# Performance work log

Hardware: AMD Instinct MI355X
Metric: run time of the kernel (lower is better)

Reference implementation:

```python
import jax, jax.numpy as jnp
import numpy as np
import math

D_MODEL = 1024
HEAD_DIM = 256
GAMMA = 0.9


def setup_inputs() -> dict:
    key = jax.random.key(0)
    k1, k2, k3, k4 = jax.random.split(key, 4)
    B, L = 4, 4096
    x = jax.random.normal(k1, (B, L, D_MODEL), dtype=jnp.float32)
    s = 1.0 / math.sqrt(D_MODEL)
    W_Q = jax.random.normal(k2, (HEAD_DIM, D_MODEL), dtype=jnp.float32) * s
    W_K = jax.random.normal(k3, (HEAD_DIM, D_MODEL), dtype=jnp.float32) * s
    W_V = jax.random.normal(k4, (HEAD_DIM, D_MODEL), dtype=jnp.float32) * s
    return {"x": x, "W_Q": W_Q, "W_K": W_K, "W_V": W_V}


def _decay_mask(L: int, gamma: float) -> jnp.ndarray:
    # D[i,j] = gamma^(i-j) if i >= j else 0
    idx = jnp.arange(L)
    diff = idx[:, None] - idx[None, :]
    return jnp.where(diff >= 0, jnp.power(jnp.float32(gamma), diff.astype(jnp.float32)), 0.0)


def reference(x, W_Q, W_K, W_V):
    B, L, _ = x.shape
    Q = jnp.einsum('bld,hd->blh', x, W_Q)  # (B,L,H)
    K = jnp.einsum('bld,hd->blh', x, W_K)
    V = jnp.einsum('bld,hd->blh', x, W_V)
    D = _decay_mask(L, GAMMA)  # (L,L)
    scores = jnp.einsum('bih,bjh->bij', Q, K) * D[None, :, :]
    scores = scores / jnp.sqrt(jnp.float32(HEAD_DIM))
    return jnp.einsum('bij,bjh->bih', scores, V)  # (B,L,H)
```

## Files before the change

### kernel.cpp

```cpp
#include <hip/hip_runtime.h>

typedef unsigned short u16;
typedef unsigned int u32;
typedef __attribute__((ext_vector_type(8))) short bf16x8;
typedef __attribute__((ext_vector_type(4))) float f32x4;
typedef __attribute__((ext_vector_type(4))) unsigned short u16x4;

#define DEVI __device__ __forceinline__

constexpr float L2GAMMA = -0.15200309344504997f;
constexpr float INV_SQRT_H = 0.0625f;

DEVI u16 f2bf(float x) {
  union { float f; unsigned u; } v; v.f = x;
  unsigned r = v.u + 0x7FFFu + ((v.u >> 16) & 1u);
  return (u16)(r >> 16);
}

DEVI u32 pack2bf(float f0, float f1) {
  u32 u0 = __float_as_uint(f0) + 0x8000u;
  u32 u1 = __float_as_uint(f1) + 0x8000u;
  return __builtin_amdgcn_perm(u1, u0, 0x07060302u);
}

__global__ void cvt_w_kernel(const float4* __restrict__ wq, const float4* __restrict__ wk,
                             const float4* __restrict__ wv, u16x4* __restrict__ dst) {
  int i = blockIdx.x * blockDim.x + threadIdx.x;
  int w = i >> 16, off = i & 65535;
  const float4* s = (w == 0) ? wq : ((w == 1) ? wk : wv);
  float4 v = s[off];
  u16x4 o; o.x = f2bf(v.x); o.y = f2bf(v.y); o.z = f2bf(v.z); o.w = f2bf(v.w);
  dst[(w << 16) + off] = o;
}

__global__ __launch_bounds__(512, 2) void qkv_gemm_kernel(const float* __restrict__ Xf, const u16* __restrict__ Wb,
                                                          u16* __restrict__ Qb, u16* __restrict__ Kb,
                                                          u16* __restrict__ Vt) {
  __shared__ u16 Alds[2][256 * 32];
  __shared__ u16 Blds[2][192 * 32];
  const int bid = blockIdx.x;
  const int xcd = bid & 7, seq = bid >> 3;
  const int m0 = (xcd * 8 + (seq >> 2)) * 256;
  const int n0 = (seq & 3) * 192;
  const int tid = threadIdx.x;
  const int wid = tid >> 6, lane = tid & 63;
  const int wm = wid >> 1, wn = wid & 1;
  const int lrow = lane & 15, lkg = lane >> 4;
  const int kidx = (lrow & 3) ^ ((lrow >> 2) & 3);
  const int kw = ((tid >> 2) & 3) ^ ((tid >> 4) & 3);
  const int kb = ((lane >> 2) & 3) ^ ((lane >> 4) & 3);

  const float* agbase = Xf + (size_t)(m0 + (tid >> 2)) * 1024 + (tid & 3) * 8;
  const int awr0 = (tid >> 2) * 32 + (((tid & 3) ^ kw) << 3);
  const int awr1 = awr0 + 128 * 32;
  float4 ar[4];

  const u16* bgbase = Wb + (size_t)(n0 + wid * 16 + (lane >> 2)) * 1024 + (((lane & 3) ^ kb) << 3);

#define LOADA(KT) do { const float* g_ = agbase + (KT) * 32; \
  ar[0] = *(const float4*)(g_); \
  ar[1] = *(const float4*)(g_ + 4); \
  ar[2] = *(const float4*)(g_ + (size_t)128 * 1024); \
  ar[3] = *(const float4*)(g_ + (size_t)128 * 1024 + 4); } while (0)

#define STAGEB(KT, BUF) do { const u16* gB_ = bgbase + (KT) * 32; \
  __builtin_amdgcn_global_load_lds((const __attribute__((address_space(1))) void*)gB_, \
      (__attribute__((address_space(3))) void*)&Blds[BUF][wid * 512], 16, 0, 0); \
  if (wid < 4) { \
    __builtin_amdgcn_global_load_lds((const __attribute__((address_space(1))) void*)(gB_ + (size_t)128 * 1024), \
        (__attribute__((address_space(3))) void*)&Blds[BUF][(8 + wid) * 512], 16, 0, 0); } } while (0)

#define CVTWRITE(BUF) do { \
  uint4 p0_, p1_; \
  p0_.x = pack2bf(ar[0].x, ar[0].y); p0_.y = pack2bf(ar[0].z, ar[0].w); \
  p0_.z = pack2bf(ar[1].x, ar[1].y); p0_.w = pack2bf(ar[1].z, ar[1].w); \
  p1_.x = pack2bf(ar[2].x, ar[2].y); p1_.y = pack2bf(ar[2].z, ar[2].w); \
  p1_.z = pack2bf(ar[3].x, ar[3].y); p1_.w = pack2bf(ar[3].z, ar[3].w); \
  *(uint4*)&Alds[BUF][awr0] = p0_; \
  *(uint4*)&Alds[BUF][awr1] = p1_; } while (0)

  f32x4 acc[4][6] = {};

  LOADA(0);
  STAGEB(0, 0);
  CVTWRITE(0);
  __syncthreads();

  for (int kt = 0; kt < 32; ++kt) {
    const int p = kt & 1;
    if (kt < 31) { LOADA(kt + 1); STAGEB(kt + 1, p ^ 1); }
    const u16* Ab = Alds[p];
    const u16* Bb = Blds[p];
    bf16x8 af[4], bfr[6];
    const int sw = (lkg ^ kidx) << 3;
#pragma unroll
    for (int mf = 0; mf < 4; ++mf) af[mf] = *(const bf16x8*)&Ab[(wm * 64 + mf * 16 + lrow) * 32 + sw];
#pragma unroll
    for (int nf = 0; nf < 6; ++nf) bfr[nf] = *(const bf16x8*)&Bb[(wn * 96 + nf * 16 + lrow) * 32 + sw];
    __builtin_amdgcn_s_setprio(1);
#pragma unroll
    for (int mf = 0; mf < 4; ++mf)
#pragma unroll
      for (int nf = 0; nf < 6; ++nf)
        acc[mf][nf] = __builtin_amdgcn_mfma_f32_16x16x32_bf16(af[mf], bfr[nf], acc[mf][nf], 0, 0, 0);
    __builtin_amdgcn_s_setprio(0);
    if (kt < 31) CVTWRITE(p ^ 1);
    __syncthreads();
  }

#pragma unroll
  for (int mf = 0; mf < 4; ++mf)
#pragma unroll
    for (int nf = 0; nf < 6; ++nf) {
      const int gm = m0 + wm * 64 + mf * 16 + lkg * 4;
      const int c = n0 + wn * 96 + nf * 16 + lrow;
      if (c < 512) {
        u16* Dst = (c < 256) ? Qb : Kb;
        const int cc = c & 255;
#pragma unroll
        for (int r = 0; r < 4; ++r) Dst[(size_t)(gm + r) * 256 + cc] = f2bf(acc[mf][nf][r]);
      } else {
        const int h = c - 512;
        const int bb = gm >> 12, l = gm & 4095;
        u16x4 pk;
        pk.x = f2bf(acc[mf][nf][0]); pk.y = f2bf(acc[mf][nf][1]);
        pk.z = f2bf(acc[mf][nf][2]); pk.w = f2bf(acc[mf][nf][3]);
        *(u16x4*)&Vt[((size_t)bb * 256 + h) * 4096 + l] = pk;
      }
    }
}

__global__ __launch_bounds__(256) void attn_kernel(const u16* __restrict__ Qb, const u16* __restrict__ Kb,
                                                   const u16* __restrict__ Vt, float* __restrict__ out) {
  __shared__ u16 Plds[32 * 72];
  const int raw = blockIdx.x;
  const int aid = (raw & 7) * 64 + (raw >> 3);
  const int b = aid >> 7;
  const int qt = aid & 127;
  const int qb = qt * 32;
  const int tid = threadIdx.x;
  const int wid = tid >> 6, lane = tid & 63;
  const int lrow = lane & 15, lkg = lane >> 4, lk = lkg * 8;
  const size_t bQK = (size_t)b * 4096 * 256;

  bf16x8 qf[2][8];
#pragma unroll
  for (int mf = 0; mf < 2; ++mf) {
    const u16* Qrow = Qb + bQK + (size_t)(qb + mf * 16 + lrow) * 256;
#pragma unroll
    for (int kf = 0; kf < 8; ++kf) qf[mf][kf] = *(const bf16x8*)&Qrow[kf * 32 + lk];
  }

  int kstart = qb - 256; if (kstart < 0) kstart = 0; kstart &= ~63;
  const int njt = (qb + 32 - kstart + 63) >> 6;

  f32x4 oacc[2][4] = {};

  for (int jt = 0; jt < njt; ++jt) {
    const int kb = kstart + jt * 64;
    f32x4 s[2] = {};
    const u16* Krow = Kb + bQK + (size_t)(kb + wid * 16 + lrow) * 256;
#pragma unroll
    for (int kf = 0; kf < 8; ++kf) {
      const bf16x8 kfr = *(const bf16x8*)&Krow[kf * 32 + lk];
      s[0] = __builtin_amdgcn_mfma_f32_16x16x32_bf16(qf[0][kf], kfr, s[0], 0, 0, 0);
      s[1] = __builtin_amdgcn_mfma_f32_16x16x32_bf16(qf[1][kf], kfr, s[1], 0, 0, 0);
    }
    const int kg = kb + wid * 16 + lrow;
#pragma unroll
    for (int mf = 0; mf < 2; ++mf) {
      const int qg = qb + mf * 16 + lkg * 4;
#pragma unroll
      for (int r = 0; r < 4; ++r) {
        const int d = qg + r - kg;
        const float pv = (d >= 0) ? s[mf][r] * exp2f((float)d * L2GAMMA) * INV_SQRT_H : 0.0f;
        Plds[(mf * 16 + lkg * 4 + r) * 72 + wid * 16 + lrow] = f2bf(pv);
      }
    }
    __syncthreads();
#pragma unroll
    for (int ks = 0; ks < 2; ++ks) {
      bf16x8 pa[2];
      pa[0] = *(const bf16x8*)&Plds[(lrow) * 72 + ks * 32 + lk];
      pa[1] = *(const bf16x8*)&Plds[(16 + lrow) * 72 + ks * 32 + lk];
#pragma unroll
      for (int nf = 0; nf < 4; ++nf) {
        const bf16x8 vb = *(const bf16x8*)&Vt[((size_t)b * 256 + wid * 64 + nf * 16 + lrow) * 4096 + kb + ks * 32 + lk];
        oacc[0][nf] = __builtin_amdgcn_mfma_f32_16x16x32_bf16(pa[0], vb, oacc[0][nf], 0, 0, 0);
        oacc[1][nf] = __builtin_amdgcn_mfma_f32_16x16x32_bf16(pa[1], vb, oacc[1][nf], 0, 0, 0);
      }
    }
    __syncthreads();
  }

#pragma unroll
  for (int mf = 0; mf < 2; ++mf) {
    float* obase = out + ((size_t)b * 4096 + qb + mf * 16 + lkg * 4) * 256 + wid * 64 + lrow;
#pragma unroll
    for (int nf = 0; nf < 4; ++nf)
#pragma unroll
      for (int r = 0; r < 4; ++r)
        obase[(size_t)r * 256 + nf * 16] = oacc[mf][nf][r];
  }
}

extern "C" void kernel_launch(void* const* d_in, const int* in_sizes, int n_in,
                              void* d_out, int out_size, void* d_ws, size_t ws_size,
                              hipStream_t stream) {
  const float* x  = (const float*)d_in[0];
  const float* wq = (const float*)d_in[1];
  const float* wk = (const float*)d_in[2];
  const float* wv = (const float*)d_in[3];
  float* out = (float*)d_out;
  char* ws = (char*)d_ws;
  u16* Wb = (u16*)(ws);
  u16* Qb = (u16*)(ws + (size_t)1572864);
  u16* Kb = (u16*)(ws + (size_t)9961472);
  u16* Vt = (u16*)(ws + (size_t)18350080);

  hipLaunchKernelGGL(cvt_w_kernel, dim3(768), dim3(256), 0, stream,
                     (const float4*)wq, (const float4*)wk, (const float4*)wv, (u16x4*)Wb);
  hipLaunchKernelGGL(qkv_gemm_kernel, dim3(256), dim3(512), 0, stream, x, Wb, Qb, Kb, Vt);
  hipLaunchKernelGGL(attn_kernel, dim3(512), dim3(256), 0, stream, Qb, Kb, Vt, out);
}
```

Baseline: 84.58 us.

## Retile QKV GEMM to 256x256 tiles with 4-stage LDS ring pipeline

The QKV projection GEMM moves from 256x192 output tiles (256 blocks) to 256x256 tiles (192 blocks), so each block produces exactly one of Q, K or V. The LDS double buffer becomes a 4-deep ring with two register sets for the fp32 X loads, keeping loads two to four k-steps ahead, and uses explicit vmcnt/lgkmcnt waits plus raw s_barrier instead of __syncthreads. The intent is to hide global-load latency better and raise MFMA work per LDS read. In exchange it uses 128KB of LDS, which limits occupancy to one block per CU, and launches fewer blocks than there are CUs.

```diff
diff --git a/kernel.cpp b/kernel.cpp
--- a/kernel.cpp
+++ b/kernel.cpp
@@ -36,98 +36,113 @@
 __global__ __launch_bounds__(512, 2) void qkv_gemm_kernel(const float* __restrict__ Xf, const u16* __restrict__ Wb,
                                                           u16* __restrict__ Qb, u16* __restrict__ Kb,
                                                           u16* __restrict__ Vt) {
-  __shared__ u16 Alds[2][256 * 32];
-  __shared__ u16 Blds[2][192 * 32];
-  const int bid = blockIdx.x;
-  const int xcd = bid & 7, seq = bid >> 3;
-  const int m0 = (xcd * 8 + (seq >> 2)) * 256;
-  const int n0 = (seq & 3) * 192;
+  __shared__ u16 lds[4][16384];
+  const int raw = blockIdx.x;
+  const int xcd = raw & 7, idx = raw >> 3;
+  const int m0 = (xcd * 8 + idx / 3) * 256;
+  const int nt = idx % 3;
+  const int n0 = nt * 256;
   const int tid = threadIdx.x;
   const int wid = tid >> 6, lane = tid & 63;
-  const int wm = wid >> 1, wn = wid & 1;
+  const int wm = wid >> 2, wn = wid & 3;
   const int lrow = lane & 15, lkg = lane >> 4;
-  const int kidx = (lrow & 3) ^ ((lrow >> 2) & 3);
-  const int kw = ((tid >> 2) & 3) ^ ((tid >> 4) & 3);
-  const int kb = ((lane >> 2) & 3) ^ ((lane >> 4) & 3);
-
-  const float* agbase = Xf + (size_t)(m0 + (tid >> 2)) * 1024 + (tid & 3) * 8;
-  const int awr0 = (tid >> 2) * 32 + (((tid & 3) ^ kw) << 3);
-  const int awr1 = awr0 + 128 * 32;
-  float4 ar[4];
-
-  const u16* bgbase = Wb + (size_t)(n0 + wid * 16 + (lane >> 2)) * 1024 + (((lane & 3) ^ kb) << 3);
-
-#define LOADA(KT) do { const float* g_ = agbase + (KT) * 32; \
-  ar[0] = *(const float4*)(g_); \
-  ar[1] = *(const float4*)(g_ + 4); \
-  ar[2] = *(const float4*)(g_ + (size_t)128 * 1024); \
-  ar[3] = *(const float4*)(g_ + (size_t)128 * 1024 + 4); } while (0)
-
-#define STAGEB(KT, BUF) do { const u16* gB_ = bgbase + (KT) * 32; \
-  __builtin_amdgcn_global_load_lds((const __attribute__((address_space(1))) void*)gB_, \
-      (__attribute__((address_space(3))) void*)&Blds[BUF][wid * 512], 16, 0, 0); \
-  if (wid < 4) { \
-    __builtin_amdgcn_global_load_lds((const __attribute__((address_space(1))) void*)(gB_ + (size_t)128 * 1024), \
-        (__attribute__((address_space(3))) void*)&Blds[BUF][(8 + wid) * 512], 16, 0, 0); } } while (0)
-
-#define CVTWRITE(BUF) do { \
-  uint4 p0_, p1_; \
-  p0_.x = pack2bf(ar[0].x, ar[0].y); p0_.y = pack2bf(ar[0].z, ar[0].w); \
-  p0_.z = pack2bf(ar[1].x, ar[1].y); p0_.w = pack2bf(ar[1].z, ar[1].w); \
-  p1_.x = pack2bf(ar[2].x, ar[2].y); p1_.y = pack2bf(ar[2].z, ar[2].w); \
-  p1_.z = pack2bf(ar[3].x, ar[3].y); p1_.w = pack2bf(ar[3].z, ar[3].w); \
-  *(uint4*)&Alds[BUF][awr0] = p0_; \
-  *(uint4*)&Alds[BUF][awr1] = p1_; } while (0)
-
-  f32x4 acc[4][6] = {};
-
-  LOADA(0);
-  STAGEB(0, 0);
-  CVTWRITE(0);
-  __syncthreads();
-
-  for (int kt = 0; kt < 32; ++kt) {
-    const int p = kt & 1;
-    if (kt < 31) { LOADA(kt + 1); STAGEB(kt + 1, p ^ 1); }
-    const u16* Ab = Alds[p];
-    const u16* Bb = Blds[p];
-    bf16x8 af[4], bfr[6];
-    const int sw = (lkg ^ kidx) << 3;
-#pragma unroll
-    for (int mf = 0; mf < 4; ++mf) af[mf] = *(const bf16x8*)&Ab[(wm * 64 + mf * 16 + lrow) * 32 + sw];
-#pragma unroll
-    for (int nf = 0; nf < 6; ++nf) bfr[nf] = *(const bf16x8*)&Bb[(wn * 96 + nf * 16 + lrow) * 32 + sw];
-    __builtin_amdgcn_s_setprio(1);
-#pragma unroll
-    for (int mf = 0; mf < 4; ++mf)
-#pragma unroll
-      for (int nf = 0; nf < 6; ++nf)
-        acc[mf][nf] = __builtin_amdgcn_mfma_f32_16x16x32_bf16(af[mf], bfr[nf], acc[mf][nf], 0, 0, 0);
-    __builtin_amdgcn_s_setprio(0);
-    if (kt < 31) CVTWRITE(p ^ 1);
-    __syncthreads();
-  }
-
-#pragma unroll
-  for (int mf = 0; mf < 4; ++mf)
-#pragma unroll
-    for (int nf = 0; nf < 6; ++nf) {
-      const int gm = m0 + wm * 64 + mf * 16 + lkg * 4;
-      const int c = n0 + wn * 96 + nf * 16 + lrow;
-      if (c < 512) {
-        u16* Dst = (c < 256) ? Qb : Kb;
-        const int cc = c & 255;
-#pragma unroll
-        for (int r = 0; r < 4; ++r) Dst[(size_t)(gm + r) * 256 + cc] = f2bf(acc[mf][nf][r]);
-      } else {
-        const int h = c - 512;
+
+#define STAGEB(T, BUF) do { const int k0_ = (T) * 32; \
+  _Pragma("unroll") for (int i_ = 0; i_ < 2; ++i_) { \
+    const int p_ = tid + i_ * 512; \
+    const int row_ = p_ >> 2; \
+    const int sc_ = ((p_ & 3) ^ ((p_ >> 4) & 3)) << 3; \
+    const u16* g_ = Wb + (size_t)(n0 + row_) * 1024 + k0_ + sc_; \
+    __builtin_amdgcn_global_load_lds((const __attribute__((address_space(1))) void*)g_, \
+        (__attribute__((address_space(3))) void*)&lds[BUF][8192 + p_ * 8], 16, 0, 0); } } while (0)
+
+#define LOADA(T, R) do { const int k0_ = (T) * 32; \
+  _Pragma("unroll") for (int i_ = 0; i_ < 2; ++i_) { \
+    const int p_ = tid + i_ * 512; \
+    const int row_ = p_ >> 2; \
+    const int sc_ = ((p_ & 3) ^ ((p_ >> 4) & 3)) << 3; \
+    const float* g_ = Xf + (size_t)(m0 + row_) * 1024 + k0_ + sc_; \
+    R[2 * i_]     = *(const float4*)g_; \
+    R[2 * i_ + 1] = *(const float4*)(g_ + 4); } } while (0)
+
+#define CVTWRITE(R, BUF) do { \
+  _Pragma("unroll") for (int i_ = 0; i_ < 2; ++i_) { \
+    const int p_ = tid + i_ * 512; \
+    uint4 pk_; \
+    pk_.x = pack2bf(R[2 * i_].x, R[2 * i_].y); \
+    pk_.y = pack2bf(R[2 * i_].z, R[2 * i_].w); \
+    pk_.z = pack2bf(R[2 * i_ + 1].x, R[2 * i_ + 1].y); \
+    pk_.w = pack2bf(R[2 * i_ + 1].z, R[2 * i_ + 1].w); \
+    *(uint4*)&lds[BUF][p_ * 8] = pk_; } } while (0)
+
+  f32x4 acc[8][4] = {};
+  float4 arE[4], arO[4];
+
+  LOADA(0, arE); LOADA(1, arO);
+  STAGEB(0, 0);  STAGEB(1, 1);
+  CVTWRITE(arE, 0); LOADA(2, arE);
+  CVTWRITE(arO, 1); LOADA(3, arO);
+  asm volatile("s_waitcnt vmcnt(8)" ::: "memory");
+  asm volatile("s_waitcnt lgkmcnt(0)" ::: "memory");
+  __builtin_amdgcn_s_barrier();
+  __builtin_amdgcn_sched_barrier(0);
+
+#define BODY(T, AR) do { \
+  const int t_ = (T); \
+  const int rb_ = t_ & 3; \
+  if (t_ + 2 < 32) STAGEB(t_ + 2, (t_ + 2) & 3); \
+  bf16x8 af_[8], bf_[4]; \
+  { const u16* Ab_ = &lds[rb_][0]; const u16* Bb_ = &lds[rb_][8192]; \
+    const int sw_ = (lkg ^ ((lrow >> 2) & 3)) << 3; \
+    _Pragma("unroll") for (int mf = 0; mf < 8; ++mf) \
+      af_[mf] = *(const bf16x8*)&Ab_[(wm * 128 + mf * 16 + lrow) * 32 + sw_]; \
+    _Pragma("unroll") for (int nf = 0; nf < 4; ++nf) \
+      bf_[nf] = *(const bf16x8*)&Bb_[(wn * 64 + nf * 16 + lrow) * 32 + sw_]; } \
+  __builtin_amdgcn_s_setprio(1); \
+  _Pragma("unroll") for (int mf = 0; mf < 8; ++mf) \
+    _Pragma("unroll") for (int nf = 0; nf < 4; ++nf) \
+      acc[mf][nf] = __builtin_amdgcn_mfma_f32_16x16x32_bf16(af_[mf], bf_[nf], acc[mf][nf], 0, 0, 0); \
+  __builtin_amdgcn_s_setprio(0); \
+  if (t_ <= 28)      { asm volatile("s_waitcnt vmcnt(6)" ::: "memory"); } \
+  else if (t_ == 29) { asm volatile("s_waitcnt vmcnt(2)" ::: "memory"); } \
+  else               { asm volatile("s_waitcnt vmcnt(0)" ::: "memory"); } \
+  if (t_ + 2 < 32) { CVTWRITE(AR, (t_ + 2) & 3); } \
+  if (t_ + 4 < 32) { LOADA(t_ + 4, AR); } \
+  asm volatile("s_waitcnt lgkmcnt(0)" ::: "memory"); \
+  __builtin_amdgcn_s_barrier(); \
+  __builtin_amdgcn_sched_barrier(0); \
+} while (0)
+
+  for (int ti = 0; ti < 16; ++ti) {
+    BODY(2 * ti, arE);
+    BODY(2 * ti + 1, arO);
+  }
+
+  if (nt < 2) {
+    u16* Dst = (nt == 0) ? Qb : Kb;
+#pragma unroll
+    for (int mf = 0; mf < 8; ++mf)
+#pragma unroll
+      for (int nf = 0; nf < 4; ++nf) {
+        const int gm = m0 + wm * 128 + mf * 16 + lkg * 4;
+        const int c = wn * 64 + nf * 16 + lrow;
+#pragma unroll
+        for (int r = 0; r < 4; ++r) Dst[(size_t)(gm + r) * 256 + c] = f2bf(acc[mf][nf][r]);
+      }
+  } else {
+#pragma unroll
+    for (int mf = 0; mf < 8; ++mf)
+#pragma unroll
+      for (int nf = 0; nf < 4; ++nf) {
+        const int gm = m0 + wm * 128 + mf * 16 + lkg * 4;
+        const int h = wn * 64 + nf * 16 + lrow;
         const int bb = gm >> 12, l = gm & 4095;
         u16x4 pk;
         pk.x = f2bf(acc[mf][nf][0]); pk.y = f2bf(acc[mf][nf][1]);
         pk.z = f2bf(acc[mf][nf][2]); pk.w = f2bf(acc[mf][nf][3]);
         *(u16x4*)&Vt[((size_t)bb * 256 + h) * 4096 + l] = pk;
       }
-    }
+  }
 }
 
 __global__ __launch_bounds__(256) void attn_kernel(const u16* __restrict__ Qb, const u16* __restrict__ Kb,
@@ -220,6 +235,6 @@
 
   hipLaunchKernelGGL(cvt_w_kernel, dim3(768), dim3(256), 0, stream,
                      (const float4*)wq, (const float4*)wk, (const float4*)wv, (u16x4*)Wb);
-  hipLaunchKernelGGL(qkv_gemm_kernel, dim3(256), dim3(512), 0, stream, x, Wb, Qb, Kb, Vt);
+  hipLaunchKernelGGL(qkv_gemm_kernel, dim3(192), dim3(512), 0, stream, x, Wb, Qb, Kb, Vt);
   hipLaunchKernelGGL(attn_kernel, dim3(512), dim3(256), 0, stream, Qb, Kb, Vt, out);
 }
```

Result: slower. 87.95 us (+4.0%).

## Retile QKV GEMM to 64-row blocks covering all 768 columns with triple-buffered weights

Applied to the files above, without the earlier changes.

The QKV projection GEMM now gives each block 64 rows of X and all 768 output columns, so every X element is read and converted to bf16 once instead of four times. Weight tiles are staged through a three-deep LDS ring using global_load_lds, with explicit vmcnt/lgkmcnt waits and a single barrier per k-step instead of __syncthreads. The cost is that every block now streams the full 1.5MB bf16 weight matrix, which puts more load on L2. The larger LDS footprint may also lower occupancy.

```diff
diff --git a/kernel.cpp b/kernel.cpp
--- a/kernel.cpp
+++ b/kernel.cpp
@@ -36,84 +36,88 @@
 __global__ __launch_bounds__(512, 2) void qkv_gemm_kernel(const float* __restrict__ Xf, const u16* __restrict__ Wb,
                                                           u16* __restrict__ Qb, u16* __restrict__ Kb,
                                                           u16* __restrict__ Vt) {
-  __shared__ u16 Alds[2][256 * 32];
-  __shared__ u16 Blds[2][192 * 32];
+  __shared__ u16 Blds[3][24576];
+  __shared__ u16 Alds[2][2048];
   const int bid = blockIdx.x;
-  const int xcd = bid & 7, seq = bid >> 3;
-  const int m0 = (xcd * 8 + (seq >> 2)) * 256;
-  const int n0 = (seq & 3) * 192;
+  const int m0 = bid << 6;
   const int tid = threadIdx.x;
   const int wid = tid >> 6, lane = tid & 63;
-  const int wm = wid >> 1, wn = wid & 1;
   const int lrow = lane & 15, lkg = lane >> 4;
-  const int kidx = (lrow & 3) ^ ((lrow >> 2) & 3);
-  const int kw = ((tid >> 2) & 3) ^ ((tid >> 4) & 3);
-  const int kb = ((lane >> 2) & 3) ^ ((lane >> 4) & 3);
-
-  const float* agbase = Xf + (size_t)(m0 + (tid >> 2)) * 1024 + (tid & 3) * 8;
-  const int awr0 = (tid >> 2) * 32 + (((tid & 3) ^ kw) << 3);
-  const int awr1 = awr0 + 128 * 32;
-  float4 ar[4];
-
-  const u16* bgbase = Wb + (size_t)(n0 + wid * 16 + (lane >> 2)) * 1024 + (((lane & 3) ^ kb) << 3);
-
-#define LOADA(KT) do { const float* g_ = agbase + (KT) * 32; \
-  ar[0] = *(const float4*)(g_); \
-  ar[1] = *(const float4*)(g_ + 4); \
-  ar[2] = *(const float4*)(g_ + (size_t)128 * 1024); \
-  ar[3] = *(const float4*)(g_ + (size_t)128 * 1024 + 4); } while (0)
-
-#define STAGEB(KT, BUF) do { const u16* gB_ = bgbase + (KT) * 32; \
-  __builtin_amdgcn_global_load_lds((const __attribute__((address_space(1))) void*)gB_, \
-      (__attribute__((address_space(3))) void*)&Blds[BUF][wid * 512], 16, 0, 0); \
-  if (wid < 4) { \
-    __builtin_amdgcn_global_load_lds((const __attribute__((address_space(1))) void*)(gB_ + (size_t)128 * 1024), \
-        (__attribute__((address_space(3))) void*)&Blds[BUF][(8 + wid) * 512], 16, 0, 0); } } while (0)
-
-#define CVTWRITE(BUF) do { \
-  uint4 p0_, p1_; \
-  p0_.x = pack2bf(ar[0].x, ar[0].y); p0_.y = pack2bf(ar[0].z, ar[0].w); \
-  p0_.z = pack2bf(ar[1].x, ar[1].y); p0_.w = pack2bf(ar[1].z, ar[1].w); \
-  p1_.x = pack2bf(ar[2].x, ar[2].y); p1_.y = pack2bf(ar[2].z, ar[2].w); \
-  p1_.z = pack2bf(ar[3].x, ar[3].y); p1_.w = pack2bf(ar[3].z, ar[3].w); \
-  *(uint4*)&Alds[BUF][awr0] = p0_; \
-  *(uint4*)&Alds[BUF][awr1] = p1_; } while (0)
+  const int brow = lane >> 2;
+  const int bcol = ((lane & 3) ^ ((lane >> 3) & 3)) << 3;
+  const int arow = tid >> 3, af4 = tid & 7;
+  const float* aload = Xf + (size_t)(m0 + arow) * 1024 + af4 * 4;
+  const int awr = arow * 32 + ((((af4 >> 1) ^ ((arow >> 1) & 3)) << 3) | ((af4 & 1) << 2));
+  const int sw = (lkg ^ ((lrow >> 1) & 3)) << 3;
+
+#define BSTAGE(T, WB) do { \
+  _Pragma("unroll") for (int j_ = 0; j_ < 6; ++j_) { \
+    const int c_ = wid * 6 + j_; \
+    const u16* g_ = Wb + (size_t)(c_ * 16 + brow) * 1024 + (T) * 32 + bcol; \
+    __builtin_amdgcn_global_load_lds((const __attribute__((address_space(1))) void*)g_, \
+        (__attribute__((address_space(3))) void*)&Blds[WB][c_ * 512], 16, 0, 0); } } while (0)
+
+#define ALOAD(T, REG) do { REG = *(const float4*)(aload + (size_t)(T) * 32); } while (0)
+
+#define ACVT(REG, AB) do { \
+  uint2 pk_; pk_.x = pack2bf(REG.x, REG.y); pk_.y = pack2bf(REG.z, REG.w); \
+  *(uint2*)&Alds[AB][awr] = pk_; } while (0)
+
+#define COMPUTE(RB, AB) do { \
+  const u16* Ab_ = Alds[AB]; const u16* Bb_ = Blds[RB]; \
+  bf16x8 af_[4], bf_[6]; \
+  _Pragma("unroll") for (int mf = 0; mf < 4; ++mf) \
+    af_[mf] = *(const bf16x8*)&Ab_[(mf * 16 + lrow) * 32 + sw]; \
+  _Pragma("unroll") for (int nf = 0; nf < 6; ++nf) \
+    bf_[nf] = *(const bf16x8*)&Bb_[(wid * 96 + nf * 16 + lrow) * 32 + sw]; \
+  __builtin_amdgcn_s_setprio(1); \
+  _Pragma("unroll") for (int mf = 0; mf < 4; ++mf) \
+    _Pragma("unroll") for (int nf = 0; nf < 6; ++nf) \
+      acc[mf][nf] = __builtin_amdgcn_mfma_f32_16x16x32_bf16(af_[mf], bf_[nf], acc[mf][nf], 0, 0, 0); \
+  __builtin_amdgcn_s_setprio(0); } while (0)
 
   f32x4 acc[4][6] = {};
-
-  LOADA(0);
-  STAGEB(0, 0);
-  CVTWRITE(0);
-  __syncthreads();
-
-  for (int kt = 0; kt < 32; ++kt) {
-    const int p = kt & 1;
-    if (kt < 31) { LOADA(kt + 1); STAGEB(kt + 1, p ^ 1); }
-    const u16* Ab = Alds[p];
-    const u16* Bb = Blds[p];
-    bf16x8 af[4], bfr[6];
-    const int sw = (lkg ^ kidx) << 3;
-#pragma unroll
-    for (int mf = 0; mf < 4; ++mf) af[mf] = *(const bf16x8*)&Ab[(wm * 64 + mf * 16 + lrow) * 32 + sw];
-#pragma unroll
-    for (int nf = 0; nf < 6; ++nf) bfr[nf] = *(const bf16x8*)&Bb[(wn * 96 + nf * 16 + lrow) * 32 + sw];
-    __builtin_amdgcn_s_setprio(1);
-#pragma unroll
-    for (int mf = 0; mf < 4; ++mf)
-#pragma unroll
-      for (int nf = 0; nf < 6; ++nf)
-        acc[mf][nf] = __builtin_amdgcn_mfma_f32_16x16x32_bf16(af[mf], bfr[nf], acc[mf][nf], 0, 0, 0);
-    __builtin_amdgcn_s_setprio(0);
-    if (kt < 31) CVTWRITE(p ^ 1);
-    __syncthreads();
+  float4 aS0, aS1;
+
+  ALOAD(0, aS0); ALOAD(1, aS1);
+  BSTAGE(0, 0); BSTAGE(1, 1);
+  ACVT(aS0, 0);
+  asm volatile("s_waitcnt vmcnt(7)" ::: "memory");
+  asm volatile("s_waitcnt lgkmcnt(0)" ::: "memory");
+  __builtin_amdgcn_s_barrier();
+
+  int rb = 0, wb = 2;
+  for (int ti = 0; ti < 16; ++ti) {
+    const bool pf = ti < 15;
+    if (pf) { ALOAD(2 * ti + 2, aS0); BSTAGE(2 * ti + 2, wb); }
+    __builtin_amdgcn_sched_barrier(0);
+    COMPUTE(rb, 0);
+    __builtin_amdgcn_sched_barrier(0);
+    ACVT(aS1, 1);
+    if (pf) { asm volatile("s_waitcnt vmcnt(7)" ::: "memory"); }
+    else    { asm volatile("s_waitcnt vmcnt(0)" ::: "memory"); }
+    asm volatile("s_waitcnt lgkmcnt(0)" ::: "memory");
+    __builtin_amdgcn_s_barrier();
+    rb = (rb == 2) ? 0 : rb + 1; wb = (wb == 2) ? 0 : wb + 1;
+    if (pf) { ALOAD(2 * ti + 3, aS1); BSTAGE(2 * ti + 3, wb); }
+    __builtin_amdgcn_sched_barrier(0);
+    COMPUTE(rb, 1);
+    __builtin_amdgcn_sched_barrier(0);
+    if (pf) {
+      ACVT(aS0, 0);
+      asm volatile("s_waitcnt vmcnt(7)" ::: "memory");
+      asm volatile("s_waitcnt lgkmcnt(0)" ::: "memory");
+      __builtin_amdgcn_s_barrier();
+    }
+    rb = (rb == 2) ? 0 : rb + 1; wb = (wb == 2) ? 0 : wb + 1;
   }
 
 #pragma unroll
   for (int mf = 0; mf < 4; ++mf)
 #pragma unroll
     for (int nf = 0; nf < 6; ++nf) {
-      const int gm = m0 + wm * 64 + mf * 16 + lkg * 4;
-      const int c = n0 + wn * 96 + nf * 16 + lrow;
+      const int gm = m0 + mf * 16 + lkg * 4;
+      const int c = wid * 96 + nf * 16 + lrow;
       if (c < 512) {
         u16* Dst = (c < 256) ? Qb : Kb;
         const int cc = c & 255;
```

Result: slower. 89.76 us (+6.1%).
